# Kernel optimization log

Measured on AMD Instinct MI355X. Metric: run time of the kernel, lower is better.

## Reference

```python
import jax, jax.numpy as jnp
import numpy as np

NUM_HEADS = 8
HIDDEN_DIM = 256
QUERY_DIM = 256
HEAD_DIM = HIDDEN_DIM // NUM_HEADS
NORM_FACT = float(HIDDEN_DIM / NUM_HEADS) ** (-0.5)


def setup_inputs() -> dict:
    key = jax.random.key(0)
    k1, k2, k3, k4, k5 = jax.random.split(key, 5)
    B, Q, H, W = 16, 100, 64, 64
    q = jax.random.normal(k1, (B, Q, QUERY_DIM), dtype=jnp.float32)
    k = jax.random.normal(k2, (B, QUERY_DIM, H, W), dtype=jnp.float32)
    mask = jax.random.randint(k3, (B, H, W), 0, 2).astype(jnp.bool_)
    # xavier_uniform for [hidden, query] linear weights
    limit = float(np.sqrt(6.0 / (HIDDEN_DIM + QUERY_DIM)))
    Wq = jax.random.uniform(k4, (HIDDEN_DIM, QUERY_DIM), minval=-limit, maxval=limit, dtype=jnp.float32)
    Wk = jax.random.uniform(k5, (HIDDEN_DIM, QUERY_DIM), minval=-limit, maxval=limit, dtype=jnp.float32)
    bq = jnp.zeros((HIDDEN_DIM,), dtype=jnp.float32)
    bk = jnp.zeros((HIDDEN_DIM,), dtype=jnp.float32)
    return {"q": q, "k": k, "Wq": Wq, "bq": bq, "Wk": Wk, "bk": bk, "mask": mask}


def reference(q, k, Wq, bq, Wk, bk, mask):
    B, Q, _ = q.shape
    _, C, H, W = k.shape
    # q projection: [B, Q, hidden]
    qp = jnp.einsum('bqc,hc->bqh', q, Wq) + bq
    # k projection via 1x1 conv == channelwise linear: [B, hidden, H, W]
    kp = jnp.einsum('bchw,oc->bohw', k, Wk) + bk[None, :, None, None]
    # split heads: qh [B,Q,nh,hd], kh [B,nh,hd,H,W]
    qh = qp.reshape(B, Q, NUM_HEADS, HEAD_DIM)
    kh = kp.reshape(B, NUM_HEADS, HEAD_DIM, H, W)
    # scores [B,Q,nh,H,W]
    weights = jnp.einsum('bqnd,bndhw->bqnhw', qh, kh) * NORM_FACT
    # masked fill: mask [B,H,W] -> broadcast over (Q, heads)
    weights = jnp.where(mask[:, None, None, :, :], -jnp.inf, weights)
    # softmax jointly over (heads, H, W), as in torch flatten(2)
    flat = weights.reshape(B, Q, NUM_HEADS * H * W)
    flat = jax.nn.softmax(flat, axis=-1)
    return flat.reshape(B, Q, NUM_HEADS, H, W)
```

## Files before the change

kernel.cpp:

```cpp
#include <hip/hip_runtime.h>
#include <hip/hip_bf16.h>
#include <math.h>

#define BB 16
#define QQ 100
#define NH 8
#define HWN 4096
#define NORM_FACT 0.17677669529663687f
#define QPAD 112

typedef short bf16x8_t __attribute__((ext_vector_type(8)));
typedef float f32x4_t  __attribute__((ext_vector_type(4)));

__device__ __forceinline__ unsigned short bf16bits(float f) {
    __hip_bfloat16 h = __float2bfloat16(f);
    return __builtin_bit_cast(unsigned short, h);
}
__device__ __forceinline__ float bf16tof(unsigned short u) {
    union { unsigned int i; float f; } x; x.i = (unsigned int)u << 16; return x.f;
}

__global__ void k_prep(const float* __restrict__ Wq, const float* __restrict__ Wk,
                       float* __restrict__ WqT, unsigned short* __restrict__ Wkbf) {
    int idx = blockIdx.x;
    int h = threadIdx.x;
    if (idx < 256) {
        WqT[idx * 256 + h] = Wq[h * 256 + idx];
    } else {
        int r = idx - 256;
        Wkbf[r * 256 + h] = bf16bits(Wk[r * 256 + h]);
    }
}

__global__ __launch_bounds__(256) void k_qproj(const float* __restrict__ q,
                                               const float* __restrict__ WqT,
                                               const float* __restrict__ bq,
                                               unsigned short* __restrict__ qphi,
                                               unsigned short* __restrict__ qplo) {
    int blk = blockIdx.x;
    int b = blk / 28, q0 = (blk % 28) * 4;
    int h = threadIdx.x;
    size_t obase = ((size_t)b * QPAD + q0) * 256 + h;
    if (q0 >= QQ) {
#pragma unroll
        for (int i = 0; i < 4; ++i) { qphi[obase + i * 256] = 0; qplo[obase + i * 256] = 0; }
        return;
    }
    __shared__ float qsh[4][256];
    int ibase = (b * QQ + q0) * 256;
#pragma unroll
    for (int i = 0; i < 4; ++i) qsh[i][h] = q[ibase + i * 256 + h];
    __syncthreads();
    float bias = bq[h];
    float a0 = bias, a1 = bias, a2 = bias, a3 = bias;
    for (int c = 0; c < 256; ++c) {
        float wv = WqT[c * 256 + h];
        a0 = fmaf(qsh[0][c], wv, a0);
        a1 = fmaf(qsh[1][c], wv, a1);
        a2 = fmaf(qsh[2][c], wv, a2);
        a3 = fmaf(qsh[3][c], wv, a3);
    }
    float a[4] = {a0 * NORM_FACT, a1 * NORM_FACT, a2 * NORM_FACT, a3 * NORM_FACT};
#pragma unroll
    for (int i = 0; i < 4; ++i) {
        unsigned short hi = bf16bits(a[i]);
        qphi[obase + i * 256] = hi;
        qplo[obase + i * 256] = bf16bits(a[i] - bf16tof(hi));
    }
}

__global__ __launch_bounds__(512) void k_kproj3(const float* __restrict__ k,
                                                const unsigned short* __restrict__ Wkbf,
                                                const float* __restrict__ bk,
                                                unsigned short* __restrict__ kpT) {
    int b = blockIdx.y;
    int hwblk = blockIdx.x * 64;
    int t = threadIdx.x;
    int w = t >> 6, lane = t & 63;
    int hwt = w & 3, oh = w >> 2;
    int n15 = lane & 15, kg = lane >> 4;
    int hw_l = hwt * 16 + n15;

    __shared__ float lds_f[64][140];

    f32x4_t acc[8];
#pragma unroll
    for (int m = 0; m < 8; ++m) acc[m] = f32x4_t{0.f, 0.f, 0.f, 0.f};

    const float* kb = k + (size_t)b * 256 * HWN + hwblk;
    const unsigned short* wbase = Wkbf + ((size_t)(oh * 128 + n15)) * 256 + kg * 8;
    int c_l = t >> 4, l16 = t & 15;

#pragma unroll
    for (int chunk = 0; chunk < 2; ++chunk) {
#pragma unroll
        for (int p = 0; p < 4; ++p) {
            int cc = p * 32 + c_l;
            float4 v = *(const float4*)(kb + (size_t)(chunk * 128 + cc) * HWN + l16 * 4);
            lds_f[l16 * 4 + 0][cc] = v.x;
            lds_f[l16 * 4 + 1][cc] = v.y;
            lds_f[l16 * 4 + 2][cc] = v.z;
            lds_f[l16 * 4 + 3][cc] = v.w;
        }
        __syncthreads();
#pragma unroll
        for (int ksl = 0; ksl < 4; ++ksl) {
            f32x4_t f0 = *(const f32x4_t*)&lds_f[hw_l][ksl * 32 + kg * 8];
            f32x4_t f1 = *(const f32x4_t*)&lds_f[hw_l][ksl * 32 + kg * 8 + 4];
            bf16x8_t bfrag;
#pragma unroll
            for (int j = 0; j < 4; ++j) {
                bfrag[j]     = (short)bf16bits(f0[j]);
                bfrag[4 + j] = (short)bf16bits(f1[j]);
            }
            int ks = chunk * 4 + ksl;
#pragma unroll
            for (int m = 0; m < 8; ++m) {
                bf16x8_t afrag = *reinterpret_cast<const bf16x8_t*>(wbase + (size_t)m * 16 * 256 + ks * 32);
                acc[m] = __builtin_amdgcn_mfma_f32_16x16x32_bf16(afrag, bfrag, acc[m], 0, 0, 0);
            }
        }
        __syncthreads();
    }

    unsigned short* tile2 = (unsigned short*)lds_f;
#pragma unroll
    for (int m = 0; m < 8; ++m) {
        ushort4 pk;
        unsigned short* pkp = (unsigned short*)&pk;
#pragma unroll
        for (int r = 0; r < 4; ++r) {
            int o = oh * 128 + m * 16 + kg * 4 + r;
            pkp[r] = bf16bits(acc[m][r] + bk[o]);
        }
        *(ushort4*)&tile2[(size_t)hw_l * 264 + oh * 128 + m * 16 + kg * 4] = pk;
    }
    __syncthreads();
    int l5 = t & 31;
#pragma unroll
    for (int it = 0; it < 4; ++it) {
        int row = it * 16 + (t >> 5);
        uint4 v = *(const uint4*)&tile2[(size_t)row * 264 + l5 * 8];
        *(uint4*)(kpT + ((size_t)b * HWN + hwblk + row) * 256 + l5 * 8) = v;
    }
}

__global__ __launch_bounds__(256) void k_sums(const unsigned short* __restrict__ qphi,
                                              const unsigned short* __restrict__ qplo,
                                              const unsigned short* __restrict__ kpT,
                                              const int* __restrict__ mask,
                                              float* __restrict__ partial) {
    int hwb = blockIdx.x, b = blockIdx.y;
    int t = threadIdx.x, w = t >> 6, lane = t & 63;
    int n15 = lane & 15, kg = lane >> 4;
    int hw = hwb * 64 + w * 16 + n15;
    float mm = mask[b * HWN + hw] ? 0.0f : 1.0f;
    const unsigned short* brow  = kpT  + ((size_t)(b * HWN + hw)) * 256 + kg * 8;
    const unsigned short* ahi_b = qphi + ((size_t)(b * QPAD + n15)) * 256 + kg * 8;
    const unsigned short* alo_b = qplo + ((size_t)(b * QPAD + n15)) * 256 + kg * 8;
    float sums[7][4] = {};
#pragma unroll 1
    for (int n = 0; n < NH; ++n) {
        bf16x8_t bfr = *reinterpret_cast<const bf16x8_t*>(brow + n * 32);
#pragma unroll
        for (int mt = 0; mt < 7; ++mt) {
            bf16x8_t ahi = *reinterpret_cast<const bf16x8_t*>(ahi_b + (size_t)(mt * 16) * 256 + n * 32);
            bf16x8_t alo = *reinterpret_cast<const bf16x8_t*>(alo_b + (size_t)(mt * 16) * 256 + n * 32);
            f32x4_t a2 = {0.f, 0.f, 0.f, 0.f};
            a2 = __builtin_amdgcn_mfma_f32_16x16x32_bf16(ahi, bfr, a2, 0, 0, 0);
            a2 = __builtin_amdgcn_mfma_f32_16x16x32_bf16(alo, bfr, a2, 0, 0, 0);
#pragma unroll
            for (int r = 0; r < 4; ++r)
                sums[mt][r] += __expf(a2[r]) * mm;
        }
    }
#pragma unroll
    for (int mt = 0; mt < 7; ++mt)
#pragma unroll
        for (int r = 0; r < 4; ++r) {
            float v = sums[mt][r];
            v += __shfl_xor(v, 1, 64);
            v += __shfl_xor(v, 2, 64);
            v += __shfl_xor(v, 4, 64);
            v += __shfl_xor(v, 8, 64);
            if (n15 == 0) {
                int qrow = mt * 16 + kg * 4 + r;
                partial[((size_t)b * QPAD + qrow) * 256 + hwb * 4 + w] = v;
            }
        }
}

__global__ __launch_bounds__(256) void k_invsum(const float* __restrict__ partial,
                                                float* __restrict__ inv) {
    int blk = blockIdx.x;
    int b = blk / QQ, qq = blk % QQ;
    const float* p = partial + ((size_t)b * QPAD + qq) * 256;
    int t = threadIdx.x;
    float v = p[t];
#pragma unroll
    for (int off = 32; off; off >>= 1) v += __shfl_xor(v, off, 64);
    __shared__ float red[4];
    if ((t & 63) == 0) red[t >> 6] = v;
    __syncthreads();
    if (t == 0) inv[blk] = 1.0f / (red[0] + red[1] + red[2] + red[3]);
}

__global__ __launch_bounds__(256) void k_write(const unsigned short* __restrict__ qphi,
                                               const unsigned short* __restrict__ qplo,
                                               const unsigned short* __restrict__ kpT,
                                               const int* __restrict__ mask,
                                               const float* __restrict__ inv,
                                               float* __restrict__ out) {
    int hws = blockIdx.x, n = blockIdx.y, b = blockIdx.z;
    int t = threadIdx.x, w = t >> 6, lane = t & 63;
    int n15 = lane & 15, kg = lane >> 4;
    int hw0 = hws * 256 + w * 64;
    float mm[4];
#pragma unroll
    for (int ht = 0; ht < 4; ++ht)
        mm[ht] = mask[b * HWN + hw0 + ht * 16 + n15] ? 0.0f : 1.0f;
    bf16x8_t bf[4];
#pragma unroll
    for (int ht = 0; ht < 4; ++ht)
        bf[ht] = *reinterpret_cast<const bf16x8_t*>(
            kpT + ((size_t)(b * HWN + hw0 + ht * 16 + n15)) * 256 + n * 32 + kg * 8);
    const unsigned short* ahi_b = qphi + ((size_t)(b * QPAD + n15)) * 256 + n * 32 + kg * 8;
    const unsigned short* alo_b = qplo + ((size_t)(b * QPAD + n15)) * 256 + n * 32 + kg * 8;
    __shared__ float lt[16][260];
#pragma unroll 1
    for (int qt = 0; qt < 7; ++qt) {
        bf16x8_t ahi = *reinterpret_cast<const bf16x8_t*>(ahi_b + (size_t)(qt * 16) * 256);
        bf16x8_t alo = *reinterpret_cast<const bf16x8_t*>(alo_b + (size_t)(qt * 16) * 256);
        float invq[4];
#pragma unroll
        for (int r = 0; r < 4; ++r) {
            int qrow = qt * 16 + kg * 4 + r;
            invq[r] = (qrow < QQ) ? inv[b * QQ + qrow] : 0.0f;
        }
#pragma unroll
        for (int ht = 0; ht < 4; ++ht) {
            f32x4_t acc = {0.f, 0.f, 0.f, 0.f};
            acc = __builtin_amdgcn_mfma_f32_16x16x32_bf16(ahi, bf[ht], acc, 0, 0, 0);
            acc = __builtin_amdgcn_mfma_f32_16x16x32_bf16(alo, bf[ht], acc, 0, 0, 0);
#pragma unroll
            for (int r = 0; r < 4; ++r)
                lt[kg * 4 + r][w * 64 + ht * 16 + n15] = __expf(acc[r]) * mm[ht] * invq[r];
        }
        __syncthreads();
#pragma unroll
        for (int j = 0; j < 4; ++j) {
            int row = w * 4 + j;
            int qrow = qt * 16 + row;
            f32x4_t v4 = *(const f32x4_t*)&lt[row][lane * 4];
            if (qrow < QQ)
                __builtin_nontemporal_store(v4,
                    (f32x4_t*)(out + (((size_t)(b * QQ + qrow)) * NH + n) * HWN + hws * 256 + lane * 4));
        }
        __syncthreads();
    }
}

extern "C" void kernel_launch(void* const* d_in, const int* in_sizes, int n_in,
                              void* d_out, int out_size, void* d_ws, size_t ws_size,
                              hipStream_t stream) {
    const float* q    = (const float*)d_in[0];
    const float* k    = (const float*)d_in[1];
    const float* Wq   = (const float*)d_in[2];
    const float* bq   = (const float*)d_in[3];
    const float* Wk   = (const float*)d_in[4];
    const float* bk   = (const float*)d_in[5];
    const int*   mask = (const int*)d_in[6];
    float* out = (float*)d_out;

    char* base = (char*)d_ws;
    unsigned short* kpT  = (unsigned short*)(base);
    unsigned short* qphi = (unsigned short*)(base + 33554432);
    unsigned short* qplo = (unsigned short*)(base + 34471936);
    float*  WqT     = (float*)(base + 35389440);
    unsigned short* Wkbf = (unsigned short*)(base + 35651584);
    float*  partial = (float*)(base + 35782656);
    float*  inv     = (float*)(base + 37617664);
    if (ws_size < (size_t)37624064) return;

    k_prep  <<<dim3(512), dim3(256), 0, stream>>>(Wq, Wk, WqT, Wkbf);
    k_qproj <<<dim3(448), dim3(256), 0, stream>>>(q, WqT, bq, qphi, qplo);
    k_kproj3<<<dim3(64, 16), dim3(512), 0, stream>>>(k, Wkbf, bk, kpT);
    k_sums  <<<dim3(64, 16), dim3(256), 0, stream>>>(qphi, qplo, kpT, mask, partial);
    k_invsum<<<dim3(1600), dim3(256), 0, stream>>>(partial, inv);
    k_write <<<dim3(16, 8, 16), dim3(256), 0, stream>>>(qphi, qplo, kpT, mask, inv, out);
}
```

Before: 193.6 us.

## Stage q tiles in LDS for sums; restructure write kernel over q-tiles with prefetch

In k_sums, the 8 head fragments of kpT are held in registers and each 16-row q tile (hi and lo) is staged cooperatively through LDS. This replaces the per-lane global loads of q that were repeated for every head. The final shuffle reduction is replaced by an LDS transpose and reduction that writes the partials. k_write now assigns one q-tile per block and loops over the 16 hw slices, software-prefetching the next kpT fragments and mask. This cuts the grid from 2048 to 896 blocks and trades parallelism for reuse of the q fragments.

```diff
diff --git a/kernel.cpp b/kernel.cpp
--- a/kernel.cpp
+++ b/kernel.cpp
@@ -155,39 +155,67 @@
     int n15 = lane & 15, kg = lane >> 4;
     int hw = hwb * 64 + w * 16 + n15;
     float mm = mask[b * HWN + hw] ? 0.0f : 1.0f;
-    const unsigned short* brow  = kpT  + ((size_t)(b * HWN + hw)) * 256 + kg * 8;
-    const unsigned short* ahi_b = qphi + ((size_t)(b * QPAD + n15)) * 256 + kg * 8;
-    const unsigned short* alo_b = qplo + ((size_t)(b * QPAD + n15)) * 256 + kg * 8;
+
+    __shared__ float ldsbuf[8960];
+    unsigned short* sA = (unsigned short*)ldsbuf;
+
+    const unsigned short* brow = kpT + ((size_t)(b * HWN + hw)) * 256 + kg * 8;
+    bf16x8_t bfr[8];
+#pragma unroll
+    for (int n = 0; n < NH; ++n)
+        bfr[n] = *reinterpret_cast<const bf16x8_t*>(brow + n * 32);
+
+    const unsigned short* ghi = qphi + (size_t)b * QPAD * 256;
+    const unsigned short* glo = qplo + (size_t)b * QPAD * 256;
+    int srow = t >> 4, schunk = t & 15;
+
     float sums[7][4] = {};
 #pragma unroll 1
-    for (int n = 0; n < NH; ++n) {
-        bf16x8_t bfr = *reinterpret_cast<const bf16x8_t*>(brow + n * 32);
-#pragma unroll
-        for (int mt = 0; mt < 7; ++mt) {
-            bf16x8_t ahi = *reinterpret_cast<const bf16x8_t*>(ahi_b + (size_t)(mt * 16) * 256 + n * 32);
-            bf16x8_t alo = *reinterpret_cast<const bf16x8_t*>(alo_b + (size_t)(mt * 16) * 256 + n * 32);
+    for (int mt = 0; mt < 7; ++mt) {
+        const unsigned short* shi = ghi + (size_t)(mt * 16 + srow) * 256 + schunk * 16;
+        const unsigned short* slo = glo + (size_t)(mt * 16 + srow) * 256 + schunk * 16;
+        uint4 vhi0 = *(const uint4*)(shi);
+        uint4 vhi1 = *(const uint4*)(shi + 8);
+        uint4 vlo0 = *(const uint4*)(slo);
+        uint4 vlo1 = *(const uint4*)(slo + 8);
+        *(uint4*)&sA[srow * 264 + schunk * 16]          = vhi0;
+        *(uint4*)&sA[srow * 264 + schunk * 16 + 8]      = vhi1;
+        *(uint4*)&sA[16 * 264 + srow * 264 + schunk * 16]     = vlo0;
+        *(uint4*)&sA[16 * 264 + srow * 264 + schunk * 16 + 8] = vlo1;
+        __syncthreads();
+#pragma unroll
+        for (int n = 0; n < NH; ++n) {
+            bf16x8_t ahi = *reinterpret_cast<const bf16x8_t*>(&sA[n15 * 264 + n * 32 + kg * 8]);
+            bf16x8_t alo = *reinterpret_cast<const bf16x8_t*>(&sA[16 * 264 + n15 * 264 + n * 32 + kg * 8]);
             f32x4_t a2 = {0.f, 0.f, 0.f, 0.f};
-            a2 = __builtin_amdgcn_mfma_f32_16x16x32_bf16(ahi, bfr, a2, 0, 0, 0);
-            a2 = __builtin_amdgcn_mfma_f32_16x16x32_bf16(alo, bfr, a2, 0, 0, 0);
+            a2 = __builtin_amdgcn_mfma_f32_16x16x32_bf16(ahi, bfr[n], a2, 0, 0, 0);
+            a2 = __builtin_amdgcn_mfma_f32_16x16x32_bf16(alo, bfr[n], a2, 0, 0, 0);
 #pragma unroll
             for (int r = 0; r < 4; ++r)
                 sums[mt][r] += __expf(a2[r]) * mm;
         }
-    }
+        __syncthreads();
+    }
+
+    float* R = ldsbuf + w * 112 * 20;
 #pragma unroll
     for (int mt = 0; mt < 7; ++mt)
 #pragma unroll
-        for (int r = 0; r < 4; ++r) {
-            float v = sums[mt][r];
-            v += __shfl_xor(v, 1, 64);
-            v += __shfl_xor(v, 2, 64);
-            v += __shfl_xor(v, 4, 64);
-            v += __shfl_xor(v, 8, 64);
-            if (n15 == 0) {
-                int qrow = mt * 16 + kg * 4 + r;
-                partial[((size_t)b * QPAD + qrow) * 256 + hwb * 4 + w] = v;
-            }
-        }
+        for (int r = 0; r < 4; ++r)
+            R[(mt * 16 + kg * 4 + r) * 20 + n15] = sums[mt][r];
+    if (lane < 56) {
+#pragma unroll
+        for (int p = 0; p < 2; ++p) {
+            int row = lane + p * 56;
+            f32x4_t v0 = *(const f32x4_t*)&R[row * 20 + 0];
+            f32x4_t v1 = *(const f32x4_t*)&R[row * 20 + 4];
+            f32x4_t v2 = *(const f32x4_t*)&R[row * 20 + 8];
+            f32x4_t v3 = *(const f32x4_t*)&R[row * 20 + 12];
+            float s = (v0[0]+v0[1]+v0[2]+v0[3]) + (v1[0]+v1[1]+v1[2]+v1[3])
+                    + (v2[0]+v2[1]+v2[2]+v2[3]) + (v3[0]+v3[1]+v3[2]+v3[3]);
+            partial[((size_t)b * QPAD + row) * 256 + hwb * 4 + w] = s;
+        }
+    }
 }
 
 __global__ __launch_bounds__(256) void k_invsum(const float* __restrict__ partial,
@@ -211,40 +239,54 @@
                                                const int* __restrict__ mask,
                                                const float* __restrict__ inv,
                                                float* __restrict__ out) {
-    int hws = blockIdx.x, n = blockIdx.y, b = blockIdx.z;
+    int qt = blockIdx.x, n = blockIdx.y, b = blockIdx.z;
     int t = threadIdx.x, w = t >> 6, lane = t & 63;
     int n15 = lane & 15, kg = lane >> 4;
-    int hw0 = hws * 256 + w * 64;
-    float mm[4];
-#pragma unroll
-    for (int ht = 0; ht < 4; ++ht)
-        mm[ht] = mask[b * HWN + hw0 + ht * 16 + n15] ? 0.0f : 1.0f;
-    bf16x8_t bf[4];
-#pragma unroll
-    for (int ht = 0; ht < 4; ++ht)
-        bf[ht] = *reinterpret_cast<const bf16x8_t*>(
-            kpT + ((size_t)(b * HWN + hw0 + ht * 16 + n15)) * 256 + n * 32 + kg * 8);
-    const unsigned short* ahi_b = qphi + ((size_t)(b * QPAD + n15)) * 256 + n * 32 + kg * 8;
-    const unsigned short* alo_b = qplo + ((size_t)(b * QPAD + n15)) * 256 + n * 32 + kg * 8;
+
+    bf16x8_t ahi = *reinterpret_cast<const bf16x8_t*>(
+        qphi + ((size_t)(b * QPAD + qt * 16 + n15)) * 256 + n * 32 + kg * 8);
+    bf16x8_t alo = *reinterpret_cast<const bf16x8_t*>(
+        qplo + ((size_t)(b * QPAD + qt * 16 + n15)) * 256 + n * 32 + kg * 8);
+    float invq[4];
+#pragma unroll
+    for (int r = 0; r < 4; ++r) {
+        int qrow = qt * 16 + kg * 4 + r;
+        invq[r] = (qrow < QQ) ? inv[b * QQ + qrow] : 0.0f;
+    }
+
     __shared__ float lt[16][260];
+
+    bf16x8_t bc[4], bn[4];
+    float mc[4], mn[4];
+#pragma unroll
+    for (int ht = 0; ht < 4; ++ht) {
+        int hw = w * 64 + ht * 16 + n15;
+        bc[ht] = *reinterpret_cast<const bf16x8_t*>(
+            kpT + ((size_t)(b * HWN + hw)) * 256 + n * 32 + kg * 8);
+        mc[ht] = mask[b * HWN + hw] ? 0.0f : 1.0f;
+        bn[ht] = bc[ht];
+        mn[ht] = mc[ht];
+    }
+
 #pragma unroll 1
-    for (int qt = 0; qt < 7; ++qt) {
-        bf16x8_t ahi = *reinterpret_cast<const bf16x8_t*>(ahi_b + (size_t)(qt * 16) * 256);
-        bf16x8_t alo = *reinterpret_cast<const bf16x8_t*>(alo_b + (size_t)(qt * 16) * 256);
-        float invq[4];
-#pragma unroll
-        for (int r = 0; r < 4; ++r) {
-            int qrow = qt * 16 + kg * 4 + r;
-            invq[r] = (qrow < QQ) ? inv[b * QQ + qrow] : 0.0f;
+    for (int hws = 0; hws < 16; ++hws) {
+        if (hws < 15) {
+#pragma unroll
+            for (int ht = 0; ht < 4; ++ht) {
+                int hw = (hws + 1) * 256 + w * 64 + ht * 16 + n15;
+                bn[ht] = *reinterpret_cast<const bf16x8_t*>(
+                    kpT + ((size_t)(b * HWN + hw)) * 256 + n * 32 + kg * 8);
+                mn[ht] = mask[b * HWN + hw] ? 0.0f : 1.0f;
+            }
         }
 #pragma unroll
         for (int ht = 0; ht < 4; ++ht) {
             f32x4_t acc = {0.f, 0.f, 0.f, 0.f};
-            acc = __builtin_amdgcn_mfma_f32_16x16x32_bf16(ahi, bf[ht], acc, 0, 0, 0);
-            acc = __builtin_amdgcn_mfma_f32_16x16x32_bf16(alo, bf[ht], acc, 0, 0, 0);
+            acc = __builtin_amdgcn_mfma_f32_16x16x32_bf16(ahi, bc[ht], acc, 0, 0, 0);
+            acc = __builtin_amdgcn_mfma_f32_16x16x32_bf16(alo, bc[ht], acc, 0, 0, 0);
 #pragma unroll
             for (int r = 0; r < 4; ++r)
-                lt[kg * 4 + r][w * 64 + ht * 16 + n15] = __expf(acc[r]) * mm[ht] * invq[r];
+                lt[kg * 4 + r][w * 64 + ht * 16 + n15] = __expf(acc[r]) * mc[ht] * invq[r];
         }
         __syncthreads();
 #pragma unroll
@@ -257,6 +299,8 @@
                     (f32x4_t*)(out + (((size_t)(b * QQ + qrow)) * NH + n) * HWN + hws * 256 + lane * 4));
         }
         __syncthreads();
+#pragma unroll
+        for (int ht = 0; ht < 4; ++ht) { bc[ht] = bn[ht]; mc[ht] = mn[ht]; }
     }
 }
 
@@ -287,5 +331,5 @@
     k_kproj3<<<dim3(64, 16), dim3(512), 0, stream>>>(k, Wkbf, bk, kpT);
     k_sums  <<<dim3(64, 16), dim3(256), 0, stream>>>(qphi, qplo, kpT, mask, partial);
     k_invsum<<<dim3(1600), dim3(256), 0, stream>>>(partial, inv);
-    k_write <<<dim3(16, 8, 16), dim3(256), 0, stream>>>(qphi, qplo, kpT, mask, inv, out);
-}
+    k_write <<<dim3(7, 8, 16), dim3(256), 0, stream>>>(qphi, qplo, kpT, mask, inv, out);
+}
```

New measurement: 192.9 us. Within noise of the previous version (-0.4%).
